# Kernel tuning notes

Hardware: AMD Instinct MI355X
Metric: run time of the kernel (lower is better)

## Reference

```python
import jax, jax.numpy as jnp
import numpy as np

N_NODES = 50000
N_GENE = 40000
N_EDGES = 800000
INPUT_DIM = 512
HID1 = 512
HID2 = 256
GOID_DIM = 4096


def setup_inputs() -> dict:
    key = jax.random.key(0)
    ks = jax.random.split(key, 20)

    def lin(k, fan_in, fan_out):
        s = 1.0 / np.sqrt(fan_in)
        kw, kb = jax.random.split(k)
        W = jax.random.uniform(kw, (fan_in, fan_out), jnp.float32, -s, s)
        b = jax.random.uniform(kb, (fan_out,), jnp.float32, -s, s)
        return W, b

    x = jax.random.normal(ks[0], (N_NODES, GOID_DIM), jnp.float32)
    edge_index = jax.random.randint(ks[1], (2, N_EDGES), 0, N_NODES, jnp.int64)
    istj = jax.random.uniform(ks[2], (N_NODES, 1), jnp.float32)

    W_go1, b_go1 = lin(ks[3], GOID_DIM, 1024)
    W_go2, b_go2 = lin(ks[4], 1024, INPUT_DIM)
    W_c1, b_c1 = lin(ks[5], INPUT_DIM, HID1)
    W_c2, b_c2 = lin(ks[6], HID1, HID2)
    W_r1, b_r1 = lin(ks[7], INPUT_DIM, HID1)
    W_r2, b_r2 = lin(ks[8], HID1, HID2)
    W_f, b_f = lin(ks[9], HID2 + 1, 2)

    return dict(x=x, edge_index=edge_index, istj=istj, n_gene=N_GENE,
                W_go1=W_go1, b_go1=b_go1, W_go2=W_go2, b_go2=b_go2,
                W_c1=W_c1, b_c1=b_c1, W_c2=W_c2, b_c2=b_c2,
                W_r1=W_r1, b_r1=b_r1, W_r2=W_r2, b_r2=b_r2,
                W_f=W_f, b_f=b_f)


def gcn_norm(edge_index, n_nodes):
    # PyG GCNConv: add self-loops, symmetric D^-1/2 (A+I) D^-1/2 normalization.
    src, dst = edge_index[0], edge_index[1]
    deg = jnp.ones((n_nodes,), jnp.float32).at[dst].add(1.0)  # self-loop + in-degree
    dinv = jax.lax.rsqrt(deg)
    edge_norm = dinv[src] * dinv[dst]          # [E]
    self_norm = dinv * dinv                    # [N], norm of self-loop edge
    return edge_norm, self_norm


def gcn_conv(h, W, b, src, dst, edge_norm, self_norm, n_nodes):
    hw = h @ W                                                     # [N, F]
    agg = jax.ops.segment_sum(edge_norm[:, None] * hw[src], dst,
                              num_segments=n_nodes)                # scatter over targets
    return agg + self_norm[:, None] * hw + b


def reference(x, edge_index, istj, n_gene,
              W_go1, b_go1, W_go2, b_go2,
              W_c1, b_c1, W_c2, b_c2,
              W_r1, b_r1, W_r2, b_r2,
              W_f, b_f):
    n_nodes = x.shape[0]
    src, dst = edge_index[0], edge_index[1]
    edge_norm, self_norm = gcn_norm(edge_index, n_nodes)

    # mask = first n_gene nodes are gene nodes (layout after torch.cat reorder)
    gene_x = x[:n_gene, :INPUT_DIM]
    goid = jax.nn.relu(x[n_gene:] @ W_go1 + b_go1)
    goid = jax.nn.relu(goid @ W_go2 + b_go2)
    xt = jnp.concatenate([gene_x, goid], axis=0)                   # [N, INPUT_DIM]

    # dropout is identity in eval mode
    h1 = jax.nn.relu(gcn_conv(xt, W_c1, b_c1, src, dst, edge_norm, self_norm, n_nodes))
    h1 = h1 + xt @ W_r1 + b_r1
    h2 = jax.nn.relu(gcn_conv(h1, W_c2, b_c2, src, dst, edge_norm, self_norm, n_nodes))
    h2 = h2 + h1 @ W_r2 + b_r2

    fusion_in = jnp.concatenate([h2[:n_gene], istj[:n_gene]], axis=1)  # [n_gene, HID2+1]
    return fusion_in @ W_f + b_f
```

## Files before the change

### kernel.cpp

```cpp
#include <hip/hip_runtime.h>

#define N_NODES 50000
#define N_GENE  40000
#define N_GOID  10000
#define N_EDGES 800000
#define GOID_DIM 4096
#define GO_HID  1024
#define D_IN    512
#define HID1    512
#define HID2    256

typedef __bf16 bf16x8 __attribute__((ext_vector_type(8)));
typedef float v4f __attribute__((ext_vector_type(4)));

__device__ __forceinline__ unsigned short f2bf(float f) {
    unsigned int u = __float_as_uint(f);
    u += 0x7FFF + ((u >> 16) & 1);
    return (unsigned short)(u >> 16);
}
__device__ __forceinline__ float b2f(unsigned short h) {
    return __uint_as_float(((unsigned int)h) << 16);
}
__device__ __forceinline__ unsigned int pack2(float a, float b) {
    return (unsigned int)f2bf(a) | ((unsigned int)f2bf(b) << 16);
}
__device__ __forceinline__ void gload_lds16(const unsigned short* g, unsigned short* l) {
    __builtin_amdgcn_global_load_lds(
        (const __attribute__((address_space(1))) unsigned int*)g,
        (__attribute__((address_space(3))) unsigned int*)l, 16, 0, 0);
}

__global__ void k_zero(int* __restrict__ p, int n) {
    int i = blockIdx.x * 256 + threadIdx.x;
    if (i < n) p[i] = 0;
}

__global__ void k_count(const int* __restrict__ dst, int* __restrict__ counts) {
    int e = blockIdx.x * 256 + threadIdx.x;
    if (e < N_EDGES) atomicAdd(&counts[dst[e]], 1);
}

__global__ __launch_bounds__(1024)
void k_scan(const int* __restrict__ counts, int* __restrict__ rowptr,
            int* __restrict__ cursor, float* __restrict__ dinv) {
    __shared__ int part[1024];
    const int CHUNK = (N_NODES + 1023) / 1024;
    int t = threadIdx.x;
    int beg = t * CHUNK;
    int end = min(beg + CHUNK, N_NODES);
    int s = 0;
    for (int i = beg; i < end; ++i) s += counts[i];
    part[t] = s;
    __syncthreads();
    for (int off = 1; off < 1024; off <<= 1) {
        int v = (t >= off) ? part[t - off] : 0;
        __syncthreads();
        part[t] += v;
        __syncthreads();
    }
    int excl = (t == 0) ? 0 : part[t - 1];
    for (int i = beg; i < end; ++i) {
        int c = counts[i];
        rowptr[i] = excl;
        cursor[i] = excl;
        dinv[i] = rsqrtf(1.0f + (float)c);
        excl += c;
    }
    if (t == 1023) rowptr[N_NODES] = part[1023];
}

__global__ void k_fill(const int* __restrict__ src, const int* __restrict__ dst,
                       int* __restrict__ cursor, int* __restrict__ csr_src) {
    int e = blockIdx.x * 256 + threadIdx.x;
    if (e < N_EDGES) {
        int d = dst[e];
        int pos = atomicAdd(&cursor[d], 1);
        csr_src[pos] = src[e];
    }
}

__global__ void k_copy_gene_bf(const float* __restrict__ x, unsigned short* __restrict__ xt) {
    int idx = blockIdx.x * 256 + threadIdx.x;
    int row = idx >> 6, c8 = (idx & 63) * 8;
    if (row >= N_GENE) return;
    const float4* s = (const float4*)(x + (size_t)row * GOID_DIM + c8);
    float4 a = s[0], b = s[1];
    uint4 u;
    u.x = pack2(a.x, a.y); u.y = pack2(a.z, a.w);
    u.z = pack2(b.x, b.y); u.w = pack2(b.z, b.w);
    *(uint4*)(xt + (size_t)row * D_IN + c8) = u;
}

__global__ void k_f2bf8(const float* __restrict__ src, unsigned short* __restrict__ dst, int n8) {
    int i = blockIdx.x * 256 + threadIdx.x;
    if (i >= n8) return;
    const float4* s = (const float4*)src;
    float4 a = s[2 * (size_t)i], b = s[2 * (size_t)i + 1];
    uint4 u;
    u.x = pack2(a.x, a.y); u.y = pack2(a.z, a.w);
    u.z = pack2(b.x, b.y); u.w = pack2(b.z, b.w);
    ((uint4*)dst)[i] = u;
}

__global__ void k_wt(const float* __restrict__ W, unsigned short* __restrict__ Wt,
                     int K, int N) {
    __shared__ float t[32][33];
    int k0 = blockIdx.y * 32, n0 = blockIdx.x * 32;
    int tx = threadIdx.x, ty = threadIdx.y;
#pragma unroll
    for (int i = 0; i < 4; ++i)
        t[ty + i * 8][tx] = W[(size_t)(k0 + ty + i * 8) * N + n0 + tx];
    __syncthreads();
#pragma unroll
    for (int i = 0; i < 4; ++i)
        Wt[(size_t)(n0 + ty + i * 8) * K + k0 + tx] = f2bf(t[tx][ty + i * 8]);
}

#define EPI_BIAS_RELU 0
#define EPI_SCALE 1
#define EPI_PLAIN 2

template <int EPI>
__global__ __launch_bounds__(256)
void k_gemm_bf(const unsigned short* __restrict__ A,
               const unsigned short* __restrict__ Bt,
               const float* __restrict__ bias,
               const float* __restrict__ rowscale,
               unsigned short* __restrict__ C,
               int M, int N, int K) {
    __shared__ unsigned short As[128 * 32];
    __shared__ unsigned short Bs[128 * 32];
    int tid = threadIdx.x;
    int l = tid & 63, w = tid >> 6;
    int bm = blockIdx.y * 128, bn = blockIdx.x * 128;

    int srow = w * 16 + (l >> 2);
    int sk = (l & 3) * 8;
    int am0 = min(bm + srow, M - 1);
    int am1 = min(bm + srow + 64, M - 1);
    const unsigned short* ag0 = A + (size_t)am0 * K + sk;
    const unsigned short* ag1 = A + (size_t)am1 * K + sk;
    const unsigned short* bg0 = Bt + (size_t)(bn + srow) * K + sk;
    const unsigned short* bg1 = Bt + (size_t)(bn + srow + 64) * K + sk;
    unsigned short* al0 = &As[w * 512];
    unsigned short* al1 = &As[2048 + w * 512];
    unsigned short* bl0 = &Bs[w * 512];
    unsigned short* bl1 = &Bs[2048 + w * 512];

    int wm = w & 1, wn = w >> 1;
    int row16 = l & 15, half = l >> 4;
    const unsigned short* Abase = &As[(wm * 64 + row16) * 32 + half * 8];
    const unsigned short* Bbase = &Bs[(wn * 64 + row16) * 32 + half * 8];

    v4f acc[4][4];
#pragma unroll
    for (int i = 0; i < 4; ++i)
#pragma unroll
        for (int j = 0; j < 4; ++j) acc[i][j] = (v4f){0.f, 0.f, 0.f, 0.f};

    for (int k0 = 0; k0 < K; k0 += 32) {
        gload_lds16(ag0, al0);
        gload_lds16(ag1, al1);
        gload_lds16(bg0, bl0);
        gload_lds16(bg1, bl1);
        ag0 += 32; ag1 += 32; bg0 += 32; bg1 += 32;
        __syncthreads();
        bf16x8 af[4], bf_[4];
#pragma unroll
        for (int t = 0; t < 4; ++t) {
            af[t] = *(const bf16x8*)(Abase + t * 16 * 32);
            bf_[t] = *(const bf16x8*)(Bbase + t * 16 * 32);
        }
#pragma unroll
        for (int i = 0; i < 4; ++i)
#pragma unroll
            for (int j = 0; j < 4; ++j)
                acc[i][j] = __builtin_amdgcn_mfma_f32_16x16x32_bf16(af[i], bf_[j], acc[i][j], 0, 0, 0);
        __syncthreads();
    }

#pragma unroll
    for (int mt = 0; mt < 4; ++mt) {
#pragma unroll
        for (int r = 0; r < 4; ++r) {
            int m = bm + wm * 64 + mt * 16 + half * 4 + r;
            if (m < M) {
                float sc = (EPI == EPI_SCALE) ? rowscale[m] : 0.f;
#pragma unroll
                for (int nt = 0; nt < 4; ++nt) {
                    int n = bn + wn * 64 + nt * 16 + row16;
                    float v = acc[mt][nt][r];
                    if (EPI == EPI_BIAS_RELU) v = fmaxf(v + bias[n], 0.f);
                    else if (EPI == EPI_SCALE) v = v * sc;
                    C[(size_t)m * N + n] = f2bf(v);
                }
            }
        }
    }
}

template <int F, bool OUT_BF16>
__global__ void k_combine(const unsigned short* __restrict__ hwS,
                          const unsigned short* __restrict__ rres,
                          const float* __restrict__ dinv,
                          const int* __restrict__ rowptr, const int* __restrict__ csr_src,
                          const float* __restrict__ bc, const float* __restrict__ br,
                          void* __restrict__ out) {
    int node = blockIdx.x;
    int c = threadIdx.x * 4;
    int beg = rowptr[node], end = rowptr[node + 1];
    ushort4 sv = *(const ushort4*)&hwS[(size_t)node * F + c];
    float a0 = b2f(sv.x), a1 = b2f(sv.y), a2 = b2f(sv.z), a3 = b2f(sv.w);
    for (int e = beg; e < end; ++e) {
        int s = csr_src[e];
        ushort4 v = *(const ushort4*)&hwS[(size_t)s * F + c];
        a0 += b2f(v.x); a1 += b2f(v.y); a2 += b2f(v.z); a3 += b2f(v.w);
    }
    float di = dinv[node];
    ushort4 rv = *(const ushort4*)&rres[(size_t)node * F + c];
    float4 vb = *(const float4*)&bc[c];
    float4 vbr = *(const float4*)&br[c];
    float o0 = fmaxf(fmaf(di, a0, vb.x), 0.f) + b2f(rv.x) + vbr.x;
    float o1 = fmaxf(fmaf(di, a1, vb.y), 0.f) + b2f(rv.y) + vbr.y;
    float o2 = fmaxf(fmaf(di, a2, vb.z), 0.f) + b2f(rv.z) + vbr.z;
    float o3 = fmaxf(fmaf(di, a3, vb.w), 0.f) + b2f(rv.w) + vbr.w;
    if (OUT_BF16) {
        unsigned short* op = (unsigned short*)out;
        ushort4 ov;
        ov.x = f2bf(o0); ov.y = f2bf(o1); ov.z = f2bf(o2); ov.w = f2bf(o3);
        *(ushort4*)&op[(size_t)node * F + c] = ov;
    } else {
        float* op = (float*)out;
        float4 ov = {o0, o1, o2, o3};
        *(float4*)&op[(size_t)node * F + c] = ov;
    }
}

__global__ __launch_bounds__(256)
void k_final(const float* __restrict__ h2, const float* __restrict__ istj,
             const float* __restrict__ Wf, const float* __restrict__ bf,
             float* __restrict__ out) {
    __shared__ float w0[257], w1[257];
    int t = threadIdx.x;
    for (int i = t; i < 257; i += 256) {
        w0[i] = Wf[2 * i];
        w1[i] = Wf[2 * i + 1];
    }
    __syncthreads();
    int wave = t >> 6, lane = t & 63;
    int row = blockIdx.x * 4 + wave;
    if (row >= N_GENE) return;
    const float4 v = *(const float4*)&h2[(size_t)row * HID2 + lane * 4];
    int c = lane * 4;
    float s0 = v.x * w0[c] + v.y * w0[c + 1] + v.z * w0[c + 2] + v.w * w0[c + 3];
    float s1 = v.x * w1[c] + v.y * w1[c + 1] + v.z * w1[c + 2] + v.w * w1[c + 3];
    for (int off = 32; off > 0; off >>= 1) {
        s0 += __shfl_down(s0, off);
        s1 += __shfl_down(s1, off);
    }
    if (lane == 0) {
        float it = istj[row];
        out[(size_t)row * 2 + 0] = s0 + it * w0[256] + bf[0];
        out[(size_t)row * 2 + 1] = s1 + it * w1[256] + bf[1];
    }
}

extern "C" void kernel_launch(void* const* d_in, const int* in_sizes, int n_in,
                              void* d_out, int out_size, void* d_ws, size_t ws_size,
                              hipStream_t stream) {
    const float* x     = (const float*)d_in[0];
    const int*   ei    = (const int*)d_in[1];
    const float* istj  = (const float*)d_in[2];
    const float* W_go1 = (const float*)d_in[4];
    const float* b_go1 = (const float*)d_in[5];
    const float* W_go2 = (const float*)d_in[6];
    const float* b_go2 = (const float*)d_in[7];
    const float* W_c1  = (const float*)d_in[8];
    const float* b_c1  = (const float*)d_in[9];
    const float* W_c2  = (const float*)d_in[10];
    const float* b_c2  = (const float*)d_in[11];
    const float* W_r1  = (const float*)d_in[12];
    const float* b_r1  = (const float*)d_in[13];
    const float* W_r2  = (const float*)d_in[14];
    const float* b_r2  = (const float*)d_in[15];
    const float* W_f   = (const float*)d_in[16];
    const float* b_f   = (const float*)d_in[17];
    float* out = (float*)d_out;

    char* w = (char*)d_ws;
    size_t off = 0;
    auto alloc = [&](size_t bytes) -> void* {
        void* p = w + off;
        off += (bytes + 255) & ~(size_t)255;
        return p;
    };
    unsigned short* xt_bf = (unsigned short*)alloc((size_t)N_NODES * D_IN * 2);
    unsigned short* bufB = (unsigned short*)alloc((size_t)N_NODES * D_IN * 2);
    unsigned short* g1_bf = bufB;
    unsigned short* bufC = (unsigned short*)alloc((size_t)N_GOID * GOID_DIM * 2);
    unsigned short* xg_bf = bufC;
    float* h2 = (float*)alloc((size_t)N_NODES * HID2 * 4);
    unsigned short* Wgo1t = (unsigned short*)alloc((size_t)GO_HID * GOID_DIM * 2);
    unsigned short* Wgo2t = (unsigned short*)alloc((size_t)D_IN * GO_HID * 2);
    unsigned short* Wc1t  = (unsigned short*)alloc((size_t)HID1 * D_IN * 2);
    unsigned short* Wr1t  = (unsigned short*)alloc((size_t)HID1 * D_IN * 2);
    unsigned short* Wc2t  = (unsigned short*)alloc((size_t)HID2 * HID1 * 2);
    unsigned short* Wr2t  = (unsigned short*)alloc((size_t)HID2 * HID1 * 2);
    float* dinv = (float*)alloc((size_t)N_NODES * 4);
    int* counts = (int*)alloc((size_t)N_NODES * 4);
    int* rowptr = (int*)alloc((size_t)(N_NODES + 1) * 4);
    int* cursor = (int*)alloc((size_t)N_NODES * 4);
    int* csr    = (int*)alloc((size_t)N_EDGES * 4);

    const int* srcp = ei;
    const int* dstp = ei + N_EDGES;

    k_zero<<<(N_NODES + 255) / 256, 256, 0, stream>>>(counts, N_NODES);
    k_count<<<(N_EDGES + 255) / 256, 256, 0, stream>>>(dstp, counts);
    k_scan<<<1, 1024, 0, stream>>>(counts, rowptr, cursor, dinv);
    k_fill<<<(N_EDGES + 255) / 256, 256, 0, stream>>>(srcp, dstp, cursor, csr);

    k_copy_gene_bf<<<(N_GENE * 64) / 256, 256, 0, stream>>>(x, xt_bf);
    k_f2bf8<<<(N_GOID * GOID_DIM / 8 + 255) / 256, 256, 0, stream>>>(
        x + (size_t)N_GENE * GOID_DIM, xg_bf, N_GOID * GOID_DIM / 8);
    k_wt<<<dim3(GO_HID / 32, GOID_DIM / 32), dim3(32, 8), 0, stream>>>(W_go1, Wgo1t, GOID_DIM, GO_HID);
    k_wt<<<dim3(D_IN / 32, GO_HID / 32), dim3(32, 8), 0, stream>>>(W_go2, Wgo2t, GO_HID, D_IN);
    k_wt<<<dim3(HID1 / 32, D_IN / 32), dim3(32, 8), 0, stream>>>(W_c1, Wc1t, D_IN, HID1);
    k_wt<<<dim3(HID1 / 32, D_IN / 32), dim3(32, 8), 0, stream>>>(W_r1, Wr1t, D_IN, HID1);
    k_wt<<<dim3(HID2 / 32, HID1 / 32), dim3(32, 8), 0, stream>>>(W_c2, Wc2t, HID1, HID2);
    k_wt<<<dim3(HID2 / 32, HID1 / 32), dim3(32, 8), 0, stream>>>(W_r2, Wr2t, HID1, HID2);

    k_gemm_bf<EPI_BIAS_RELU><<<dim3(GO_HID / 128, (N_GOID + 127) / 128), 256, 0, stream>>>(
        xg_bf, Wgo1t, b_go1, nullptr, g1_bf, N_GOID, GO_HID, GOID_DIM);
    k_gemm_bf<EPI_BIAS_RELU><<<dim3(D_IN / 128, (N_GOID + 127) / 128), 256, 0, stream>>>(
        g1_bf, Wgo2t, b_go2, nullptr, xt_bf + (size_t)N_GENE * D_IN, N_GOID, D_IN, GO_HID);

    k_gemm_bf<EPI_SCALE><<<dim3(HID1 / 128, (N_NODES + 127) / 128), 256, 0, stream>>>(
        xt_bf, Wc1t, nullptr, dinv, bufB, N_NODES, HID1, D_IN);
    k_gemm_bf<EPI_PLAIN><<<dim3(HID1 / 128, (N_NODES + 127) / 128), 256, 0, stream>>>(
        xt_bf, Wr1t, nullptr, nullptr, bufC, N_NODES, HID1, D_IN);
    k_combine<HID1, true><<<N_NODES, HID1 / 4, 0, stream>>>(
        bufB, bufC, dinv, rowptr, csr, b_c1, b_r1, xt_bf);

    k_gemm_bf<EPI_SCALE><<<dim3(HID2 / 128, (N_NODES + 127) / 128), 256, 0, stream>>>(
        xt_bf, Wc2t, nullptr, dinv, bufB, N_NODES, HID2, HID1);
    k_gemm_bf<EPI_PLAIN><<<dim3(HID2 / 128, (N_NODES + 127) / 128), 256, 0, stream>>>(
        xt_bf, Wr2t, nullptr, nullptr, bufC, N_NODES, HID2, HID1);
    k_combine<HID2, false><<<N_NODES, HID2 / 4, 0, stream>>>(
        bufB, bufC, dinv, rowptr, csr, b_c2, b_r2, h2);

    k_final<<<(N_GENE + 3) / 4, 256, 0, stream>>>(h2, istj, W_f, b_f, out);
}
```

Before: 1.746 ms.

## Fuse conv and residual GEMMs, fuse final linear into layer-2 combine

Concatenates the conv and residual weights so each layer runs one GEMM with doubled N, sharing the A-tile loads, and splits the output into the scaled conv buffer and the plain residual buffer. The layer-2 combine is fused with the final 257->2 linear, which removes the fp32 h2 buffer and a kernel launch. Only gene nodes are aggregated in layer 2, and residual tiles for non-gene rows are skipped. The layer-1 combine now uses 8-wide loads with a 2-way unrolled gather. Risks include extra branching in the GEMM epilogue.

Measured after the change: 1.729 ms. No clear change (-1.0%).

```diff
diff --git a/kernel.cpp b/kernel.cpp
--- a/kernel.cpp
+++ b/kernel.cpp
@@ -23,6 +23,10 @@
 }
 __device__ __forceinline__ unsigned int pack2(float a, float b) {
     return (unsigned int)f2bf(a) | ((unsigned int)f2bf(b) << 16);
+}
+__device__ __forceinline__ void unp2(unsigned int u, float& lo, float& hi) {
+    lo = __uint_as_float(u << 16);
+    hi = __uint_as_float(u & 0xffff0000u);
 }
 __device__ __forceinline__ void gload_lds16(const unsigned short* g, unsigned short* l) {
     __builtin_amdgcn_global_load_lds(
@@ -117,8 +121,7 @@
 }
 
 #define EPI_BIAS_RELU 0
-#define EPI_SCALE 1
-#define EPI_PLAIN 2
+#define EPI_CONV 1
 
 template <int EPI>
 __global__ __launch_bounds__(256)
@@ -127,12 +130,17 @@
                const float* __restrict__ bias,
                const float* __restrict__ rowscale,
                unsigned short* __restrict__ C,
-               int M, int N, int K) {
+               unsigned short* __restrict__ C2,
+               int M, int N, int K, int NH, int Mr) {
     __shared__ unsigned short As[128 * 32];
     __shared__ unsigned short Bs[128 * 32];
     int tid = threadIdx.x;
     int l = tid & 63, w = tid >> 6;
     int bm = blockIdx.y * 128, bn = blockIdx.x * 128;
+
+    if (EPI == EPI_CONV) {
+        if (bn >= NH && bm >= Mr) return;
+    }
 
     int srow = w * 16 + (l >> 2);
     int sk = (l & 3) * 8;
@@ -185,83 +193,139 @@
         for (int r = 0; r < 4; ++r) {
             int m = bm + wm * 64 + mt * 16 + half * 4 + r;
             if (m < M) {
-                float sc = (EPI == EPI_SCALE) ? rowscale[m] : 0.f;
+                float sc = (EPI == EPI_CONV) ? rowscale[m] : 0.f;
 #pragma unroll
                 for (int nt = 0; nt < 4; ++nt) {
                     int n = bn + wn * 64 + nt * 16 + row16;
                     float v = acc[mt][nt][r];
-                    if (EPI == EPI_BIAS_RELU) v = fmaxf(v + bias[n], 0.f);
-                    else if (EPI == EPI_SCALE) v = v * sc;
-                    C[(size_t)m * N + n] = f2bf(v);
+                    if (EPI == EPI_BIAS_RELU) {
+                        v = fmaxf(v + bias[n], 0.f);
+                        C[(size_t)m * N + n] = f2bf(v);
+                    } else {
+                        if (n < NH)
+                            C[(size_t)m * NH + n] = f2bf(v * sc);
+                        else
+                            C2[(size_t)m * NH + (n - NH)] = f2bf(v);
+                    }
                 }
             }
         }
     }
 }
 
-template <int F, bool OUT_BF16>
-__global__ void k_combine(const unsigned short* __restrict__ hwS,
-                          const unsigned short* __restrict__ rres,
-                          const float* __restrict__ dinv,
-                          const int* __restrict__ rowptr, const int* __restrict__ csr_src,
-                          const float* __restrict__ bc, const float* __restrict__ br,
-                          void* __restrict__ out) {
+__global__ void k_combine512(const unsigned short* __restrict__ hwS,
+                             const unsigned short* __restrict__ rres,
+                             const float* __restrict__ dinv,
+                             const int* __restrict__ rowptr, const int* __restrict__ csr_src,
+                             const float* __restrict__ bc, const float* __restrict__ br,
+                             unsigned short* __restrict__ out) {
     int node = blockIdx.x;
-    int c = threadIdx.x * 4;
+    int c = threadIdx.x * 8;
     int beg = rowptr[node], end = rowptr[node + 1];
-    ushort4 sv = *(const ushort4*)&hwS[(size_t)node * F + c];
-    float a0 = b2f(sv.x), a1 = b2f(sv.y), a2 = b2f(sv.z), a3 = b2f(sv.w);
-    for (int e = beg; e < end; ++e) {
-        int s = csr_src[e];
-        ushort4 v = *(const ushort4*)&hwS[(size_t)s * F + c];
-        a0 += b2f(v.x); a1 += b2f(v.y); a2 += b2f(v.z); a3 += b2f(v.w);
+    uint4 sv = *(const uint4*)(hwS + (size_t)node * HID1 + c);
+    float a0, a1, a2, a3, a4, a5, a6, a7;
+    unp2(sv.x, a0, a1); unp2(sv.y, a2, a3); unp2(sv.z, a4, a5); unp2(sv.w, a6, a7);
+    int e = beg;
+    for (; e + 2 <= end; e += 2) {
+        int s0 = csr_src[e], s1 = csr_src[e + 1];
+        uint4 v0 = *(const uint4*)(hwS + (size_t)s0 * HID1 + c);
+        uint4 v1 = *(const uint4*)(hwS + (size_t)s1 * HID1 + c);
+        float t0, t1;
+        unp2(v0.x, t0, t1); a0 += t0; a1 += t1;
+        unp2(v0.y, t0, t1); a2 += t0; a3 += t1;
+        unp2(v0.z, t0, t1); a4 += t0; a5 += t1;
+        unp2(v0.w, t0, t1); a6 += t0; a7 += t1;
+        unp2(v1.x, t0, t1); a0 += t0; a1 += t1;
+        unp2(v1.y, t0, t1); a2 += t0; a3 += t1;
+        unp2(v1.z, t0, t1); a4 += t0; a5 += t1;
+        unp2(v1.w, t0, t1); a6 += t0; a7 += t1;
+    }
+    if (e < end) {
+        int s0 = csr_src[e];
+        uint4 v0 = *(const uint4*)(hwS + (size_t)s0 * HID1 + c);
+        float t0, t1;
+        unp2(v0.x, t0, t1); a0 += t0; a1 += t1;
+        unp2(v0.y, t0, t1); a2 += t0; a3 += t1;
+        unp2(v0.z, t0, t1); a4 += t0; a5 += t1;
+        unp2(v0.w, t0, t1); a6 += t0; a7 += t1;
     }
     float di = dinv[node];
-    ushort4 rv = *(const ushort4*)&rres[(size_t)node * F + c];
+    uint4 rv = *(const uint4*)(rres + (size_t)node * HID1 + c);
+    float r0, r1, r2, r3, r4, r5, r6, r7;
+    unp2(rv.x, r0, r1); unp2(rv.y, r2, r3); unp2(rv.z, r4, r5); unp2(rv.w, r6, r7);
+    float4 vb0 = *(const float4*)&bc[c];
+    float4 vb1 = *(const float4*)&bc[c + 4];
+    float4 vq0 = *(const float4*)&br[c];
+    float4 vq1 = *(const float4*)&br[c + 4];
+    float o0 = fmaxf(fmaf(di, a0, vb0.x), 0.f) + r0 + vq0.x;
+    float o1 = fmaxf(fmaf(di, a1, vb0.y), 0.f) + r1 + vq0.y;
+    float o2 = fmaxf(fmaf(di, a2, vb0.z), 0.f) + r2 + vq0.z;
+    float o3 = fmaxf(fmaf(di, a3, vb0.w), 0.f) + r3 + vq0.w;
+    float o4 = fmaxf(fmaf(di, a4, vb1.x), 0.f) + r4 + vq1.x;
+    float o5 = fmaxf(fmaf(di, a5, vb1.y), 0.f) + r5 + vq1.y;
+    float o6 = fmaxf(fmaf(di, a6, vb1.z), 0.f) + r6 + vq1.z;
+    float o7 = fmaxf(fmaf(di, a7, vb1.w), 0.f) + r7 + vq1.w;
+    uint4 ov;
+    ov.x = pack2(o0, o1); ov.y = pack2(o2, o3);
+    ov.z = pack2(o4, o5); ov.w = pack2(o6, o7);
+    *(uint4*)(out + (size_t)node * HID1 + c) = ov;
+}
+
+__global__ void k_combine_final(const unsigned short* __restrict__ hwS,
+                                const unsigned short* __restrict__ rres,
+                                const float* __restrict__ dinv,
+                                const int* __restrict__ rowptr, const int* __restrict__ csr_src,
+                                const float* __restrict__ bc, const float* __restrict__ br,
+                                const float* __restrict__ istj,
+                                const float* __restrict__ Wf, const float* __restrict__ bfv,
+                                float* __restrict__ out) {
+    int node = blockIdx.x;
+    int t = threadIdx.x;
+    int c = t * 4;
+    int beg = rowptr[node], end = rowptr[node + 1];
+    uint2 sv = *(const uint2*)(hwS + (size_t)node * HID2 + c);
+    float a0, a1, a2, a3;
+    unp2(sv.x, a0, a1); unp2(sv.y, a2, a3);
+    int e = beg;
+    for (; e + 2 <= end; e += 2) {
+        int s0 = csr_src[e], s1 = csr_src[e + 1];
+        uint2 v0 = *(const uint2*)(hwS + (size_t)s0 * HID2 + c);
+        uint2 v1 = *(const uint2*)(hwS + (size_t)s1 * HID2 + c);
+        float t0, t1;
+        unp2(v0.x, t0, t1); a0 += t0; a1 += t1;
+        unp2(v0.y, t0, t1); a2 += t0; a3 += t1;
+        unp2(v1.x, t0, t1); a0 += t0; a1 += t1;
+        unp2(v1.y, t0, t1); a2 += t0; a3 += t1;
+    }
+    if (e < end) {
+        int s0 = csr_src[e];
+        uint2 v0 = *(const uint2*)(hwS + (size_t)s0 * HID2 + c);
+        float t0, t1;
+        unp2(v0.x, t0, t1); a0 += t0; a1 += t1;
+        unp2(v0.y, t0, t1); a2 += t0; a3 += t1;
+    }
+    float di = dinv[node];
+    uint2 rv = *(const uint2*)(rres + (size_t)node * HID2 + c);
+    float r0, r1, r2, r3;
+    unp2(rv.x, r0, r1); unp2(rv.y, r2, r3);
     float4 vb = *(const float4*)&bc[c];
-    float4 vbr = *(const float4*)&br[c];
-    float o0 = fmaxf(fmaf(di, a0, vb.x), 0.f) + b2f(rv.x) + vbr.x;
-    float o1 = fmaxf(fmaf(di, a1, vb.y), 0.f) + b2f(rv.y) + vbr.y;
-    float o2 = fmaxf(fmaf(di, a2, vb.z), 0.f) + b2f(rv.z) + vbr.z;
-    float o3 = fmaxf(fmaf(di, a3, vb.w), 0.f) + b2f(rv.w) + vbr.w;
-    if (OUT_BF16) {
-        unsigned short* op = (unsigned short*)out;
-        ushort4 ov;
-        ov.x = f2bf(o0); ov.y = f2bf(o1); ov.z = f2bf(o2); ov.w = f2bf(o3);
-        *(ushort4*)&op[(size_t)node * F + c] = ov;
-    } else {
-        float* op = (float*)out;
-        float4 ov = {o0, o1, o2, o3};
-        *(float4*)&op[(size_t)node * F + c] = ov;
-    }
-}
-
-__global__ __launch_bounds__(256)
-void k_final(const float* __restrict__ h2, const float* __restrict__ istj,
-             const float* __restrict__ Wf, const float* __restrict__ bf,
-             float* __restrict__ out) {
-    __shared__ float w0[257], w1[257];
-    int t = threadIdx.x;
-    for (int i = t; i < 257; i += 256) {
-        w0[i] = Wf[2 * i];
-        w1[i] = Wf[2 * i + 1];
-    }
-    __syncthreads();
-    int wave = t >> 6, lane = t & 63;
-    int row = blockIdx.x * 4 + wave;
-    if (row >= N_GENE) return;
-    const float4 v = *(const float4*)&h2[(size_t)row * HID2 + lane * 4];
-    int c = lane * 4;
-    float s0 = v.x * w0[c] + v.y * w0[c + 1] + v.z * w0[c + 2] + v.w * w0[c + 3];
-    float s1 = v.x * w1[c] + v.y * w1[c + 1] + v.z * w1[c + 2] + v.w * w1[c + 3];
+    float4 vq = *(const float4*)&br[c];
+    float o0 = fmaxf(fmaf(di, a0, vb.x), 0.f) + r0 + vq.x;
+    float o1 = fmaxf(fmaf(di, a1, vb.y), 0.f) + r1 + vq.y;
+    float o2 = fmaxf(fmaf(di, a2, vb.z), 0.f) + r2 + vq.z;
+    float o3 = fmaxf(fmaf(di, a3, vb.w), 0.f) + r3 + vq.w;
+    float4 wa = *(const float4*)&Wf[2 * c];
+    float4 wb = *(const float4*)&Wf[2 * c + 4];
+    float s0 = o0 * wa.x + o1 * wa.z + o2 * wb.x + o3 * wb.z;
+    float s1 = o0 * wa.y + o1 * wa.w + o2 * wb.y + o3 * wb.w;
     for (int off = 32; off > 0; off >>= 1) {
         s0 += __shfl_down(s0, off);
         s1 += __shfl_down(s1, off);
     }
-    if (lane == 0) {
-        float it = istj[row];
-        out[(size_t)row * 2 + 0] = s0 + it * w0[256] + bf[0];
-        out[(size_t)row * 2 + 1] = s1 + it * w1[256] + bf[1];
+    if (t == 0) {
+        float it = istj[node];
+        out[(size_t)node * 2 + 0] = s0 + it * Wf[2 * HID2] + bfv[0];
+        out[(size_t)node * 2 + 1] = s1 + it * Wf[2 * HID2 + 1] + bfv[1];
     }
 }
 
@@ -299,13 +363,10 @@
     unsigned short* g1_bf = bufB;
     unsigned short* bufC = (unsigned short*)alloc((size_t)N_GOID * GOID_DIM * 2);
     unsigned short* xg_bf = bufC;
-    float* h2 = (float*)alloc((size_t)N_NODES * HID2 * 4);
     unsigned short* Wgo1t = (unsigned short*)alloc((size_t)GO_HID * GOID_DIM * 2);
     unsigned short* Wgo2t = (unsigned short*)alloc((size_t)D_IN * GO_HID * 2);
-    unsigned short* Wc1t  = (unsigned short*)alloc((size_t)HID1 * D_IN * 2);
-    unsigned short* Wr1t  = (unsigned short*)alloc((size_t)HID1 * D_IN * 2);
-    unsigned short* Wc2t  = (unsigned short*)alloc((size_t)HID2 * HID1 * 2);
-    unsigned short* Wr2t  = (unsigned short*)alloc((size_t)HID2 * HID1 * 2);
+    unsigned short* Wcr1t = (unsigned short*)alloc((size_t)(2 * HID1) * D_IN * 2);
+    unsigned short* Wcr2t = (unsigned short*)alloc((size_t)(2 * HID2) * HID1 * 2);
     float* dinv = (float*)alloc((size_t)N_NODES * 4);
     int* counts = (int*)alloc((size_t)N_NODES * 4);
     int* rowptr = (int*)alloc((size_t)(N_NODES + 1) * 4);
@@ -325,29 +386,27 @@
         x + (size_t)N_GENE * GOID_DIM, xg_bf, N_GOID * GOID_DIM / 8);
     k_wt<<<dim3(GO_HID / 32, GOID_DIM / 32), dim3(32, 8), 0, stream>>>(W_go1, Wgo1t, GOID_DIM, GO_HID);
     k_wt<<<dim3(D_IN / 32, GO_HID / 32), dim3(32, 8), 0, stream>>>(W_go2, Wgo2t, GO_HID, D_IN);
-    k_wt<<<dim3(HID1 / 32, D_IN / 32), dim3(32, 8), 0, stream>>>(W_c1, Wc1t, D_IN, HID1);
-    k_wt<<<dim3(HID1 / 32, D_IN / 32), dim3(32, 8), 0, stream>>>(W_r1, Wr1t, D_IN, HID1);
-    k_wt<<<dim3(HID2 / 32, HID1 / 32), dim3(32, 8), 0, stream>>>(W_c2, Wc2t, HID1, HID2);
-    k_wt<<<dim3(HID2 / 32, HID1 / 32), dim3(32, 8), 0, stream>>>(W_r2, Wr2t, HID1, HID2);
+    k_wt<<<dim3(HID1 / 32, D_IN / 32), dim3(32, 8), 0, stream>>>(W_c1, Wcr1t, D_IN, HID1);
+    k_wt<<<dim3(HID1 / 32, D_IN / 32), dim3(32, 8), 0, stream>>>(
+        W_r1, Wcr1t + (size_t)HID1 * D_IN, D_IN, HID1);
+    k_wt<<<dim3(HID2 / 32, HID1 / 32), dim3(32, 8), 0, stream>>>(W_c2, Wcr2t, HID1, HID2);
+    k_wt<<<dim3(HID2 / 32, HID1 / 32), dim3(32, 8), 0, stream>>>(
+        W_r2, Wcr2t + (size_t)HID2 * HID1, HID1, HID2);
 
     k_gemm_bf<EPI_BIAS_RELU><<<dim3(GO_HID / 128, (N_GOID + 127) / 128), 256, 0, stream>>>(
-        xg_bf, Wgo1t, b_go1, nullptr, g1_bf, N_GOID, GO_HID, GOID_DIM);
+        xg_bf, Wgo1t, b_go1, nullptr, g1_bf, nullptr, N_GOID, GO_HID, GOID_DIM, 0, 0);
     k_gemm_bf<EPI_BIAS_RELU><<<dim3(D_IN / 128, (N_GOID + 127) / 128), 256, 0, stream>>>(
-        g1_bf, Wgo2t, b_go2, nullptr, xt_bf + (size_t)N_GENE * D_IN, N_GOID, D_IN, GO_HID);
-
-    k_gemm_bf<EPI_SCALE><<<dim3(HID1 / 128, (N_NODES + 127) / 128), 256, 0, stream>>>(
-        xt_bf, Wc1t, nullptr, dinv, bufB, N_NODES, HID1, D_IN);
-    k_gemm_bf<EPI_PLAIN><<<dim3(HID1 / 128, (N_NODES + 127) / 128), 256, 0, stream>>>(
-        xt_bf, Wr1t, nullptr, nullptr, bufC, N_NODES, HID1, D_IN);
-    k_combine<HID1, true><<<N_NODES, HID1 / 4, 0, stream>>>(
+        g1_bf, Wgo2t, b_go2, nullptr, xt_bf + (size_t)N_GENE * D_IN, nullptr,
+        N_GOID, D_IN, GO_HID, 0, 0);
+
+    k_gemm_bf<EPI_CONV><<<dim3(2 * HID1 / 128, (N_NODES + 127) / 128), 256, 0, stream>>>(
+        xt_bf, Wcr1t, nullptr, dinv, bufB, bufC, N_NODES, 2 * HID1, D_IN, HID1, N_NODES);
+    k_combine512<<<N_NODES, HID1 / 8, 0, stream>>>(
         bufB, bufC, dinv, rowptr, csr, b_c1, b_r1, xt_bf);
 
-    k_gemm_bf<EPI_SCALE><<<dim3(HID2 / 128, (N_NODES + 127) / 128), 256, 0, stream>>>(
-        xt_bf, Wc2t, nullptr, dinv, bufB, N_NODES, HID2, HID1);
-    k_gemm_bf<EPI_PLAIN><<<dim3(HID2 / 128, (N_NODES + 127) / 128), 256, 0, stream>>>(
-        xt_bf, Wr2t, nullptr, nullptr, bufC, N_NODES, HID2, HID1);
-    k_combine<HID2, false><<<N_NODES, HID2 / 4, 0, stream>>>(
-        bufB, bufC, dinv, rowptr, csr, b_c2, b_r2, h2);
-
-    k_final<<<(N_GENE + 3) / 4, 256, 0, stream>>>(h2, istj, W_f, b_f, out);
-}
+    k_gemm_bf<EPI_CONV><<<dim3(2 * HID2 / 128, (N_NODES + 127) / 128), 256, 0, stream>>>(
+        xt_bf, Wcr2t, nullptr, dinv, bufB, bufC, N_NODES, 2 * HID2, HID1, HID2, N_GENE);
+
+    k_combine_final<<<N_GENE, HID2 / 4, 0, stream>>>(
+        bufB, bufC, dinv, rowptr, csr, b_c2, b_r2, istj, W_f, b_f, out);
+}
```
